# Kernel optimization log

Measured on AMD Instinct MI355X. Metric: run time of the kernel, lower is better.

Reference implementation:

```python
import jax, jax.numpy as jnp
import numpy as np

# FlowNetC correlation config (kernel_size=1 -> pointwise patch; pad == max_displacement)
PAD = 20
MAX_DISP = 20
STRIDE2 = 2


def setup_inputs() -> dict:
    key = jax.random.key(0)
    k1, k2 = jax.random.split(key)
    B, C, H, W = 4, 256, 96, 96
    input1 = jax.random.normal(k1, (B, C, H, W), dtype=jnp.float32)
    input2 = jax.random.normal(k2, (B, C, H, W), dtype=jnp.float32)
    return {"input1": input1, "input2": input2}


def _correlation(x1, x2):
    # x1, x2: [B, C, H, W]. Output: [B, D*D, H, W] with D = 2*MAX_DISP//STRIDE2 + 1.
    B, C, H, W = x1.shape
    x2p = jnp.pad(x2, ((0, 0), (0, 0), (PAD, PAD), (PAD, PAD)))
    D = 2 * MAX_DISP // STRIDE2 + 1  # 21
    # start index into padded map = PAD + (disp) where disp = off - MAX_DISP;
    # since PAD == MAX_DISP, start index == off.
    offs = jnp.arange(D, dtype=jnp.int32) * STRIDE2
    dyv, dxv = jnp.meshgrid(offs, offs, indexing="ij")
    pairs = jnp.stack([dyv.ravel(), dxv.ravel()], axis=1)  # [D*D, 2]
    inv_c = jnp.float32(1.0 / C)  # CUDA kernel divides by kernel^2 * C (kernel=1)

    def body(_, p):
        dy, dx = p[0], p[1]
        sl = jax.lax.dynamic_slice(x2p, (0, 0, dy, dx), (B, C, H, W))
        return None, jnp.einsum("bchw,bchw->bhw", x1, sl) * inv_c

    _, corr = jax.lax.scan(body, None, pairs)  # [D*D, B, H, W]
    return corr.transpose(1, 0, 2, 3)  # [B, D*D, H, W]


def reference(input1, input2):
    return _correlation(input1, input2)
```

## Files before the change

### kernel.cpp

```cpp
#include <hip/hip_runtime.h>
#include <hip/hip_bf16.h>


typedef __bf16 bf16x8 __attribute__((ext_vector_type(8)));
typedef float f32x4 __attribute__((ext_vector_type(4)));

#define B_ 4
#define C_ 256
#define H_ 96
#define W_ 96
#define NOFF 21
#define ROWS 96
#define IMG_ELEMS (ROWS * C_)
#define IMG_BYTES (IMG_ELEMS * 2)
#define X1T_ELEMS (B_ * H_ * IMG_ELEMS)

__device__ __forceinline__ unsigned short f32_to_bf16_rne(float f) {
    union { float f; unsigned u; } v; v.f = f;
    unsigned u = v.u;
    return (unsigned short)((u + 0x7fffu + ((u >> 16) & 1u)) >> 16);
}

__device__ __forceinline__ void gl2lds16(const void* g, void* l) {
    __builtin_amdgcn_global_load_lds(
        (const __attribute__((address_space(1))) void*)g,
        (__attribute__((address_space(3))) void*)l, 16, 0, 0);
}

__global__ __launch_bounds__(256) void prep_kernel(const float* __restrict__ x1,
                                                   const float* __restrict__ x2,
                                                   unsigned short* __restrict__ ws) {
    __shared__ float tile[96 * 65];
    int bid = blockIdx.x;
    int cblk  = bid & 3;
    int which = (bid >> 2) & 1;
    int bh    = bid >> 3;
    int h = bh % H_;
    int b = bh / H_;
    int c0 = cblk << 6;

    const float* src = (which ? x2 : x1) + ((size_t)(b * C_ + c0) * H_ + h) * W_;
    unsigned short* dst = ws + (size_t)which * X1T_ELEMS + (size_t)(b * H_ + h) * IMG_ELEMS;

    for (int idx = threadIdx.x; idx < 64 * 96; idx += 256) {
        int c = idx / 96, w = idx - c * 96;
        tile[w * 65 + c] = src[c * (H_ * W_) + w];
    }
    __syncthreads();

    for (int idx = threadIdx.x; idx < 96 * 8; idx += 256) {
        int row = idx >> 3, tp = idx & 7;
        int par = row / 48, i = row - par * 48;
        int w = 2 * i + par;
        int s = tp ^ (row & 7);
        const float* fsrc = &tile[w * 65 + (s << 3)];
        unsigned pk[4];
#pragma unroll
        for (int e = 0; e < 4; ++e) {
            unsigned lo = f32_to_bf16_rne(fsrc[2 * e]);
            unsigned hi = f32_to_bf16_rne(fsrc[2 * e + 1]);
            pk[e] = lo | (hi << 16);
        }
        int ccp = (((c0 >> 3) ^ (row & 24)) + tp);
        *(uint4*)((char*)(dst + (size_t)row * C_) + (ccp << 4)) =
            make_uint4(pk[0], pk[1], pk[2], pk[3]);
    }
}

__global__ __launch_bounds__(384, 1) void corr_kernel(const unsigned short* __restrict__ ws,
                                                      float* __restrict__ out) {
    __shared__ unsigned short Bs[3][IMG_ELEMS];
    __shared__ float sl[NOFF][97];
    static_assert(sizeof(Bs) + sizeof(sl) <= 163840, "LDS budget");

    int bid = blockIdx.x;
    int xcd = bid & 7, sidx = bid >> 3;
    int b  = xcd >> 1;
    int h  = ((xcd & 1) ? 48 : 0) + (sidx >> 1);
    int og = sidx & 1;

    int tid = threadIdx.x;
    int wv = tid >> 6, lane = tid & 63;
    int par = wv & 1, mt = wv >> 1;
    int i0 = mt << 4;
    int n = lane & 15, quad = lane >> 4;

    int rowA = par * 48 + i0 + n;
    const unsigned short* Ag = ws + (size_t)(b * H_ + h) * IMG_ELEMS + (size_t)rowA * C_;
    int keyA = rowA & 31;
    bf16x8 afrag[8];
#pragma unroll
    for (int ks = 0; ks < 8; ++ks)
        afrag[ks] = *(const bf16x8*)(Ag + ((((ks << 2) | quad) ^ keyA) << 3));

    const unsigned short* Bimg = ws + (size_t)X1T_ELEMS + (size_t)(b * H_) * IMG_ELEMS;

    int rowB0 = par * 48 + n;
    int rowB1 = rowB0 + 16;
    int rowB2 = rowB0 + 32;
    int keyB0 = rowB0 & 31, keyB1 = rowB1 & 31, keyB2 = rowB2 & 31;

    int oy_lo = og ? 11 : 0;
    int oy_hi = og ? NOFF : 11;

    int vlo = oy_lo, vhi = oy_hi;
    {
        int lo = (h <= 20) ? ((21 - h) >> 1) : 0;
        int hi = ((115 - h) >> 1) + 1;
        if (lo > vlo) vlo = lo;
        if (hi < vhi) vhi = hi;
    }
    int nv = vhi - vlo; if (nv < 0) nv = 0;

    int wvoff  = wv * 8192;
    int gmaoff = wvoff + lane * 16;

    if (nv > 0) {
        const char* Bg = (const char*)(Bimg + (size_t)(h + 2 * vlo - 20) * IMG_ELEMS);
#pragma unroll
        for (int c = 0; c < 8; ++c)
            gl2lds16(Bg + gmaoff + c * 1024, (char*)Bs[0] + wvoff + c * 1024);
    }
    if (nv > 1) {
        const char* Bg = (const char*)(Bimg + (size_t)(h + 2 * (vlo + 1) - 20) * IMG_ELEMS);
#pragma unroll
        for (int c = 0; c < 8; ++c)
            gl2lds16(Bg + gmaoff + c * 1024, (char*)Bs[1] + wvoff + c * 1024);
    }

    for (int oy = oy_lo; oy < oy_hi; ++oy) {
        if (oy >= vlo && oy < vhi) continue;
        int outb = ((b * 441 + oy * NOFF) * H_ + h) * W_;
        for (int idx = tid; idx < NOFF * W_; idx += 384)
            out[outb + (idx / W_) * (H_ * W_) + (idx % W_)] = 0.0f;
    }

    for (int k = 0; k < nv; ++k) {
        int oy = vlo + k;
        int cur = k % 3;

        if (k + 2 < nv) {
            int nb = (k + 2) % 3;
            const char* Bg = (const char*)(Bimg + (size_t)(h + 2 * (oy + 2) - 20) * IMG_ELEMS);
#pragma unroll
            for (int c = 0; c < 8; ++c)
                gl2lds16(Bg + gmaoff + c * 1024, (char*)Bs[nb] + wvoff + c * 1024);
        }

        if (k == 0) {
            if (nv > 2)       asm volatile("s_waitcnt vmcnt(16)\ns_barrier" ::: "memory");
            else if (nv == 2) asm volatile("s_waitcnt vmcnt(8)\ns_barrier" ::: "memory");
            else              asm volatile("s_waitcnt vmcnt(0)\ns_barrier" ::: "memory");
        } else if (k + 2 < nv) {
            asm volatile("s_waitcnt vmcnt(21)\ns_barrier" ::: "memory");
        } else if (k + 1 < nv) {
            asm volatile("s_waitcnt vmcnt(13)\ns_barrier" ::: "memory");
        } else {
            asm volatile("s_waitcnt vmcnt(5)\ns_barrier" ::: "memory");
        }

        f32x4 acc0 = {0.f,0.f,0.f,0.f}, acc1 = {0.f,0.f,0.f,0.f}, acc2 = {0.f,0.f,0.f,0.f};
        const char* Bsb = (const char*)Bs[cur];
        if (mt == 0) {
#pragma unroll
            for (int ks = 0; ks < 8; ++ks) {
                int ci = (ks << 2) | quad;
                bf16x8 b0 = *(const bf16x8*)(Bsb + rowB0 * 512 + ((ci ^ keyB0) << 4));
                bf16x8 b1 = *(const bf16x8*)(Bsb + rowB1 * 512 + ((ci ^ keyB1) << 4));
                acc0 = __builtin_amdgcn_mfma_f32_16x16x32_bf16(afrag[ks], b0, acc0, 0, 0, 0);
                acc1 = __builtin_amdgcn_mfma_f32_16x16x32_bf16(afrag[ks], b1, acc1, 0, 0, 0);
            }
        } else if (mt == 1) {
#pragma unroll
            for (int ks = 0; ks < 8; ++ks) {
                int ci = (ks << 2) | quad;
                bf16x8 b0 = *(const bf16x8*)(Bsb + rowB0 * 512 + ((ci ^ keyB0) << 4));
                bf16x8 b1 = *(const bf16x8*)(Bsb + rowB1 * 512 + ((ci ^ keyB1) << 4));
                bf16x8 b2 = *(const bf16x8*)(Bsb + rowB2 * 512 + ((ci ^ keyB2) << 4));
                acc0 = __builtin_amdgcn_mfma_f32_16x16x32_bf16(afrag[ks], b0, acc0, 0, 0, 0);
                acc1 = __builtin_amdgcn_mfma_f32_16x16x32_bf16(afrag[ks], b1, acc1, 0, 0, 0);
                acc2 = __builtin_amdgcn_mfma_f32_16x16x32_bf16(afrag[ks], b2, acc2, 0, 0, 0);
            }
        } else {
#pragma unroll
            for (int ks = 0; ks < 8; ++ks) {
                int ci = (ks << 2) | quad;
                bf16x8 b1 = *(const bf16x8*)(Bsb + rowB1 * 512 + ((ci ^ keyB1) << 4));
                bf16x8 b2 = *(const bf16x8*)(Bsb + rowB2 * 512 + ((ci ^ keyB2) << 4));
                acc1 = __builtin_amdgcn_mfma_f32_16x16x32_bf16(afrag[ks], b1, acc1, 0, 0, 0);
                acc2 = __builtin_amdgcn_mfma_f32_16x16x32_bf16(afrag[ks], b2, acc2, 0, 0, 0);
            }
        }

#pragma unroll
        for (int r = 0; r < 4; ++r) {
            int m = (quad << 2) + r;
            int w = 2 * (i0 + m) + par;
            int oxb = n - i0 - m - 6;
            if (mt != 2) { int ox = 16 + oxb; if (ox >= 0 && ox < NOFF) sl[ox][w] = acc0[r]; }
            {             int ox = 32 + oxb; if (ox >= 0 && ox < NOFF) sl[ox][w] = acc1[r]; }
            if (mt != 0) { int ox = 48 + oxb; if (ox >= 0 && ox < NOFF) sl[ox][w] = acc2[r]; }
        }

        asm volatile("s_waitcnt lgkmcnt(0)\ns_barrier" ::: "memory");

        int outb = ((b * 441 + oy * NOFF) * H_ + h) * W_;
        for (int idx = tid; idx < NOFF * W_; idx += 384) {
            int ox = idx / W_, w = idx - ox * W_;
            int w2 = w + 2 * ox - 20;
            float v = (w2 >= 0 && w2 < W_) ? sl[ox][w] * (1.0f / 256.0f) : 0.0f;
            out[outb + ox * (H_ * W_) + w] = v;
        }
    }
}

__global__ __launch_bounds__(256) void corr_fallback(const float* __restrict__ x1,
                                                     const float* __restrict__ x2,
                                                     float* __restrict__ out) {
    int bid = blockIdx.x;
    int oy = bid % NOFF, h = (bid / NOFF) % H_, b = bid / (NOFF * H_);
    int dy = 2 * oy - 20, h2 = h + dy;
    int outbase = ((b * 441 + oy * NOFF) * H_ + h) * W_;
    for (int idx = threadIdx.x; idx < NOFF * W_; idx += 256) {
        int ox = idx / W_, w = idx % W_;
        float acc = 0.f;
        int w2 = w + 2 * ox - 20;
        if (h2 >= 0 && h2 < H_ && w2 >= 0 && w2 < W_) {
            const float* p1 = x1 + (size_t)b * C_ * H_ * W_ + h * W_ + w;
            const float* p2 = x2 + (size_t)b * C_ * H_ * W_ + h2 * W_ + w2;
            for (int c = 0; c < C_; ++c) acc += p1[c * (H_ * W_)] * p2[c * (H_ * W_)];
        }
        out[outbase + ox * (H_ * W_) + w] = acc * (1.0f / 256.0f);
    }
}

extern "C" void kernel_launch(void* const* d_in, const int* in_sizes, int n_in,
                              void* d_out, int out_size, void* d_ws, size_t ws_size,
                              hipStream_t stream) {
    const float* x1 = (const float*)d_in[0];
    const float* x2 = (const float*)d_in[1];
    float* out = (float*)d_out;

    size_t need = (size_t)2 * X1T_ELEMS * sizeof(unsigned short);
    if (ws_size >= need) {
        unsigned short* ws = (unsigned short*)d_ws;
        prep_kernel<<<B_ * H_ * 2 * 4, 256, 0, stream>>>(x1, x2, ws);
        corr_kernel<<<768, 384, 0, stream>>>(ws, out);
    } else {
        corr_fallback<<<B_ * H_ * NOFF, 256, 0, stream>>>(x1, x2, out);
    }
}
```

Measured before the change: 178.2 us.

## Share each loaded x2 row image across two output rows h and h+2

Each block now handles two output rows (hA and hA+2) that share the same shifted x2 row images, so each LDS-staged B tile feeds MFMAs for both rows. The displacement range is split into four groups instead of two, and the output store loop is precomputed per thread with fixed slot and offset tables. This halves B-tile global-to-LDS traffic per output and raises MFMA work per barrier. In exchange it doubles the A fragments held in registers and the LDS staging buffer, and launch bounds now request two blocks per CU, which may not fit the register or LDS budget.

```diff
diff --git a/kernel.cpp b/kernel.cpp
--- a/kernel.cpp
+++ b/kernel.cpp
@@ -12,7 +12,6 @@
 #define NOFF 21
 #define ROWS 96
 #define IMG_ELEMS (ROWS * C_)
-#define IMG_BYTES (IMG_ELEMS * 2)
 #define X1T_ELEMS (B_ * H_ * IMG_ELEMS)
 
 __device__ __forceinline__ unsigned short f32_to_bf16_rne(float f) {
@@ -67,17 +66,21 @@
     }
 }
 
-__global__ __launch_bounds__(384, 1) void corr_kernel(const unsigned short* __restrict__ ws,
+__global__ __launch_bounds__(384, 2) void corr_kernel(const unsigned short* __restrict__ ws,
                                                       float* __restrict__ out) {
     __shared__ unsigned short Bs[3][IMG_ELEMS];
-    __shared__ float sl[NOFF][97];
+    __shared__ float sl[2][NOFF][97];
     static_assert(sizeof(Bs) + sizeof(sl) <= 163840, "LDS budget");
 
     int bid = blockIdx.x;
     int xcd = bid & 7, sidx = bid >> 3;
     int b  = xcd >> 1;
-    int h  = ((xcd & 1) ? 48 : 0) + (sidx >> 1);
-    int og = sidx & 1;
+    int p  = ((xcd & 1) ? 24 : 0) + (sidx >> 2);
+    int og = sidx & 3;
+    int g = p >> 1, par_h = p & 1;
+    int hA = 4 * g + par_h, hB = hA + 2;
+    int olo = (og * NOFF) >> 2;
+    int ohi = ((og + 1) * NOFF) >> 2;
 
     int tid = threadIdx.x;
     int wv = tid >> 6, lane = tid & 63;
@@ -85,13 +88,29 @@
     int i0 = mt << 4;
     int n = lane & 15, quad = lane >> 4;
 
+    int jcnt = 5 + (tid < 96 ? 1 : 0);
+    int slotj[6], offj[6]; bool mj[6];
+#pragma unroll
+    for (int j = 0; j < 6; ++j) {
+        int idx = tid + j * 384;
+        int ox = idx / W_, w = idx - ox * W_;
+        slotj[j] = ox * 97 + w;
+        offj[j]  = ox * (H_ * W_) + w;
+        int w2 = w + 2 * ox - 20;
+        mj[j] = (w2 >= 0) & (w2 < W_);
+    }
+
     int rowA = par * 48 + i0 + n;
-    const unsigned short* Ag = ws + (size_t)(b * H_ + h) * IMG_ELEMS + (size_t)rowA * C_;
     int keyA = rowA & 31;
-    bf16x8 afrag[8];
-#pragma unroll
-    for (int ks = 0; ks < 8; ++ks)
-        afrag[ks] = *(const bf16x8*)(Ag + ((((ks << 2) | quad) ^ keyA) << 3));
+    const unsigned short* AgA = ws + (size_t)(b * H_ + hA) * IMG_ELEMS + (size_t)rowA * C_;
+    const unsigned short* AgB = ws + (size_t)(b * H_ + hB) * IMG_ELEMS + (size_t)rowA * C_;
+    bf16x8 afA[8], afB[8];
+#pragma unroll
+    for (int ks = 0; ks < 8; ++ks) {
+        int o = (((ks << 2) | quad) ^ keyA) << 3;
+        afA[ks] = *(const bf16x8*)(AgA + o);
+        afB[ks] = *(const bf16x8*)(AgB + o);
+    }
 
     const unsigned short* Bimg = ws + (size_t)X1T_ELEMS + (size_t)(b * H_) * IMG_ELEMS;
 
@@ -100,48 +119,63 @@
     int rowB2 = rowB0 + 32;
     int keyB0 = rowB0 & 31, keyB1 = rowB1 & 31, keyB2 = rowB2 & 31;
 
-    int oy_lo = og ? 11 : 0;
-    int oy_hi = og ? NOFF : 11;
-
-    int vlo = oy_lo, vhi = oy_hi;
-    {
-        int lo = (h <= 20) ? ((21 - h) >> 1) : 0;
-        int hi = ((115 - h) >> 1) + 1;
-        if (lo > vlo) vlo = lo;
-        if (hi < vhi) vhi = hi;
-    }
-    int nv = vhi - vlo; if (nv < 0) nv = 0;
+    int aLo = (hA <= 20) ? ((21 - hA) >> 1) : 0; if (aLo < olo) aLo = olo;
+    int aHi = ((115 - hA) >> 1) + 1;             if (aHi > ohi) aHi = ohi;
+    if (aHi < aLo) aHi = aLo;
+    int bLo = (hB <= 20) ? ((21 - hB) >> 1) : 0; if (bLo < olo) bLo = olo;
+    int bHi = ((115 - hB) >> 1) + 1;             if (bHi > ohi) bHi = ohi;
+    if (bHi < bLo) bHi = bLo;
+
+    int tlo, thi;
+    bool ea = (aLo >= aHi), eb = (bLo >= bHi);
+    if (ea && eb)      { tlo = 0; thi = 0; }
+    else if (ea)       { tlo = bLo + 1; thi = bHi + 1; }
+    else if (eb)       { tlo = aLo; thi = aHi; }
+    else {
+        tlo = (aLo < bLo + 1) ? aLo : bLo + 1;
+        thi = (aHi > bHi + 1) ? aHi : bHi + 1;
+    }
+    int nv = thi - tlo;
 
     int wvoff  = wv * 8192;
     int gmaoff = wvoff + lane * 16;
 
     if (nv > 0) {
-        const char* Bg = (const char*)(Bimg + (size_t)(h + 2 * vlo - 20) * IMG_ELEMS);
+        const char* Bg = (const char*)(Bimg + (size_t)(hA + 2 * tlo - 20) * IMG_ELEMS);
 #pragma unroll
         for (int c = 0; c < 8; ++c)
             gl2lds16(Bg + gmaoff + c * 1024, (char*)Bs[0] + wvoff + c * 1024);
     }
     if (nv > 1) {
-        const char* Bg = (const char*)(Bimg + (size_t)(h + 2 * (vlo + 1) - 20) * IMG_ELEMS);
+        const char* Bg = (const char*)(Bimg + (size_t)(hA + 2 * (tlo + 1) - 20) * IMG_ELEMS);
 #pragma unroll
         for (int c = 0; c < 8; ++c)
             gl2lds16(Bg + gmaoff + c * 1024, (char*)Bs[1] + wvoff + c * 1024);
     }
 
-    for (int oy = oy_lo; oy < oy_hi; ++oy) {
-        if (oy >= vlo && oy < vhi) continue;
-        int outb = ((b * 441 + oy * NOFF) * H_ + h) * W_;
-        for (int idx = tid; idx < NOFF * W_; idx += 384)
-            out[outb + (idx / W_) * (H_ * W_) + (idx % W_)] = 0.0f;
-    }
+    for (int oy = olo; oy < ohi; ++oy) {
+        if (oy < aLo || oy >= aHi) {
+            int outb = ((b * 441 + oy * NOFF) * H_ + hA) * W_;
+#pragma unroll
+            for (int j = 0; j < 6; ++j) if (j < jcnt) out[outb + offj[j]] = 0.0f;
+        }
+        if (oy < bLo || oy >= bHi) {
+            int outb = ((b * 441 + oy * NOFF) * H_ + hB) * W_;
+#pragma unroll
+            for (int j = 0; j < 6; ++j) if (j < jcnt) out[outb + offj[j]] = 0.0f;
+        }
+    }
+
+    const float* slA = &sl[0][0][0];
+    const float* slB = &sl[1][0][0];
 
     for (int k = 0; k < nv; ++k) {
-        int oy = vlo + k;
+        int t = tlo + k;
         int cur = k % 3;
 
         if (k + 2 < nv) {
             int nb = (k + 2) % 3;
-            const char* Bg = (const char*)(Bimg + (size_t)(h + 2 * (oy + 2) - 20) * IMG_ELEMS);
+            const char* Bg = (const char*)(Bimg + (size_t)(hA + 2 * (t + 2) - 20) * IMG_ELEMS);
 #pragma unroll
             for (int c = 0; c < 8; ++c)
                 gl2lds16(Bg + gmaoff + c * 1024, (char*)Bs[nb] + wvoff + c * 1024);
@@ -159,36 +193,57 @@
             asm volatile("s_waitcnt vmcnt(5)\ns_barrier" ::: "memory");
         }
 
-        f32x4 acc0 = {0.f,0.f,0.f,0.f}, acc1 = {0.f,0.f,0.f,0.f}, acc2 = {0.f,0.f,0.f,0.f};
         const char* Bsb = (const char*)Bs[cur];
+        f32x4 aA0 = {0.f,0.f,0.f,0.f}, aA1 = {0.f,0.f,0.f,0.f}, aA2 = {0.f,0.f,0.f,0.f};
+        f32x4 aB0 = {0.f,0.f,0.f,0.f}, aB1 = {0.f,0.f,0.f,0.f}, aB2 = {0.f,0.f,0.f,0.f};
+
         if (mt == 0) {
+            bf16x8 f0[8], f1[8];
 #pragma unroll
             for (int ks = 0; ks < 8; ++ks) {
                 int ci = (ks << 2) | quad;
-                bf16x8 b0 = *(const bf16x8*)(Bsb + rowB0 * 512 + ((ci ^ keyB0) << 4));
-                bf16x8 b1 = *(const bf16x8*)(Bsb + rowB1 * 512 + ((ci ^ keyB1) << 4));
-                acc0 = __builtin_amdgcn_mfma_f32_16x16x32_bf16(afrag[ks], b0, acc0, 0, 0, 0);
-                acc1 = __builtin_amdgcn_mfma_f32_16x16x32_bf16(afrag[ks], b1, acc1, 0, 0, 0);
+                f0[ks] = *(const bf16x8*)(Bsb + rowB0 * 512 + ((ci ^ keyB0) << 4));
+                f1[ks] = *(const bf16x8*)(Bsb + rowB1 * 512 + ((ci ^ keyB1) << 4));
+            }
+#pragma unroll
+            for (int ks = 0; ks < 8; ++ks) {
+                aA0 = __builtin_amdgcn_mfma_f32_16x16x32_bf16(afA[ks], f0[ks], aA0, 0, 0, 0);
+                aA1 = __builtin_amdgcn_mfma_f32_16x16x32_bf16(afA[ks], f1[ks], aA1, 0, 0, 0);
+                aB0 = __builtin_amdgcn_mfma_f32_16x16x32_bf16(afB[ks], f0[ks], aB0, 0, 0, 0);
+                aB1 = __builtin_amdgcn_mfma_f32_16x16x32_bf16(afB[ks], f1[ks], aB1, 0, 0, 0);
             }
         } else if (mt == 1) {
+            bf16x8 f0[8], f1[8], f2[8];
 #pragma unroll
             for (int ks = 0; ks < 8; ++ks) {
                 int ci = (ks << 2) | quad;
-                bf16x8 b0 = *(const bf16x8*)(Bsb + rowB0 * 512 + ((ci ^ keyB0) << 4));
-                bf16x8 b1 = *(const bf16x8*)(Bsb + rowB1 * 512 + ((ci ^ keyB1) << 4));
-                bf16x8 b2 = *(const bf16x8*)(Bsb + rowB2 * 512 + ((ci ^ keyB2) << 4));
-                acc0 = __builtin_amdgcn_mfma_f32_16x16x32_bf16(afrag[ks], b0, acc0, 0, 0, 0);
-                acc1 = __builtin_amdgcn_mfma_f32_16x16x32_bf16(afrag[ks], b1, acc1, 0, 0, 0);
-                acc2 = __builtin_amdgcn_mfma_f32_16x16x32_bf16(afrag[ks], b2, acc2, 0, 0, 0);
+                f0[ks] = *(const bf16x8*)(Bsb + rowB0 * 512 + ((ci ^ keyB0) << 4));
+                f1[ks] = *(const bf16x8*)(Bsb + rowB1 * 512 + ((ci ^ keyB1) << 4));
+                f2[ks] = *(const bf16x8*)(Bsb + rowB2 * 512 + ((ci ^ keyB2) << 4));
+            }
+#pragma unroll
+            for (int ks = 0; ks < 8; ++ks) {
+                aA0 = __builtin_amdgcn_mfma_f32_16x16x32_bf16(afA[ks], f0[ks], aA0, 0, 0, 0);
+                aA1 = __builtin_amdgcn_mfma_f32_16x16x32_bf16(afA[ks], f1[ks], aA1, 0, 0, 0);
+                aA2 = __builtin_amdgcn_mfma_f32_16x16x32_bf16(afA[ks], f2[ks], aA2, 0, 0, 0);
+                aB0 = __builtin_amdgcn_mfma_f32_16x16x32_bf16(afB[ks], f0[ks], aB0, 0, 0, 0);
+                aB1 = __builtin_amdgcn_mfma_f32_16x16x32_bf16(afB[ks], f1[ks], aB1, 0, 0, 0);
+                aB2 = __builtin_amdgcn_mfma_f32_16x16x32_bf16(afB[ks], f2[ks], aB2, 0, 0, 0);
             }
         } else {
+            bf16x8 f1[8], f2[8];
 #pragma unroll
             for (int ks = 0; ks < 8; ++ks) {
                 int ci = (ks << 2) | quad;
-                bf16x8 b1 = *(const bf16x8*)(Bsb + rowB1 * 512 + ((ci ^ keyB1) << 4));
-                bf16x8 b2 = *(const bf16x8*)(Bsb + rowB2 * 512 + ((ci ^ keyB2) << 4));
-                acc1 = __builtin_amdgcn_mfma_f32_16x16x32_bf16(afrag[ks], b1, acc1, 0, 0, 0);
-                acc2 = __builtin_amdgcn_mfma_f32_16x16x32_bf16(afrag[ks], b2, acc2, 0, 0, 0);
+                f1[ks] = *(const bf16x8*)(Bsb + rowB1 * 512 + ((ci ^ keyB1) << 4));
+                f2[ks] = *(const bf16x8*)(Bsb + rowB2 * 512 + ((ci ^ keyB2) << 4));
+            }
+#pragma unroll
+            for (int ks = 0; ks < 8; ++ks) {
+                aA1 = __builtin_amdgcn_mfma_f32_16x16x32_bf16(afA[ks], f1[ks], aA1, 0, 0, 0);
+                aA2 = __builtin_amdgcn_mfma_f32_16x16x32_bf16(afA[ks], f2[ks], aA2, 0, 0, 0);
+                aB1 = __builtin_amdgcn_mfma_f32_16x16x32_bf16(afB[ks], f1[ks], aB1, 0, 0, 0);
+                aB2 = __builtin_amdgcn_mfma_f32_16x16x32_bf16(afB[ks], f2[ks], aB2, 0, 0, 0);
             }
         }
 
@@ -197,19 +252,31 @@
             int m = (quad << 2) + r;
             int w = 2 * (i0 + m) + par;
             int oxb = n - i0 - m - 6;
-            if (mt != 2) { int ox = 16 + oxb; if (ox >= 0 && ox < NOFF) sl[ox][w] = acc0[r]; }
-            {             int ox = 32 + oxb; if (ox >= 0 && ox < NOFF) sl[ox][w] = acc1[r]; }
-            if (mt != 0) { int ox = 48 + oxb; if (ox >= 0 && ox < NOFF) sl[ox][w] = acc2[r]; }
+            if (mt != 2) { int ox = 16 + oxb; if (ox >= 0 && ox < NOFF) { sl[0][ox][w] = aA0[r]; sl[1][ox][w] = aB0[r]; } }
+            {             int ox = 32 + oxb; if (ox >= 0 && ox < NOFF) { sl[0][ox][w] = aA1[r]; sl[1][ox][w] = aB1[r]; } }
+            if (mt != 0) { int ox = 48 + oxb; if (ox >= 0 && ox < NOFF) { sl[0][ox][w] = aA2[r]; sl[1][ox][w] = aB2[r]; } }
         }
 
         asm volatile("s_waitcnt lgkmcnt(0)\ns_barrier" ::: "memory");
 
-        int outb = ((b * 441 + oy * NOFF) * H_ + h) * W_;
-        for (int idx = tid; idx < NOFF * W_; idx += 384) {
-            int ox = idx / W_, w = idx - ox * W_;
-            int w2 = w + 2 * ox - 20;
-            float v = (w2 >= 0 && w2 < W_) ? sl[ox][w] * (1.0f / 256.0f) : 0.0f;
-            out[outb + ox * (H_ * W_) + w] = v;
+        bool okA = (t >= aLo) & (t < aHi);
+        bool okB = (t - 1 >= bLo) & (t - 1 < bHi);
+        int outbA = ((b * 441 + t * NOFF) * H_ + hA) * W_;
+        int outbB = ((b * 441 + (t - 1) * NOFF) * H_ + hB) * W_;
+
+        float vA[6], vB[6];
+#pragma unroll
+        for (int j = 0; j < 6; ++j) if (j < jcnt) {
+            vA[j] = mj[j] ? slA[slotj[j]] * (1.0f / 256.0f) : 0.0f;
+            vB[j] = mj[j] ? slB[slotj[j]] * (1.0f / 256.0f) : 0.0f;
+        }
+        if (okA) {
+#pragma unroll
+            for (int j = 0; j < 6; ++j) if (j < jcnt) out[outbA + offj[j]] = vA[j];
+        }
+        if (okB) {
+#pragma unroll
+            for (int j = 0; j < 6; ++j) if (j < jcnt) out[outbB + offj[j]] = vB[j];
         }
     }
 }
```

Result: faster. 164.6 us (-7.6%).
